# Kernel tuning notes

Measured on AMD Instinct MI355X. Metric: run time of the kernel, lower is better.

## Reference

```python
import jax, jax.numpy as jnp
import numpy as np

N_INPUT = 32
N_NEURONS = 64
N_OUTPUT = 16
BATCH = 2_000_000


def setup_inputs() -> dict:
    key = jax.random.key(0)
    k_in, k0, k1, k2 = jax.random.split(key, 4)
    inputs = jax.random.normal(k_in, (BATCH, N_INPUT), dtype=jnp.float32)
    # torch.nn.Linear(in, out, bias=False) weights have shape [out, in],
    # init U(-1/sqrt(in), 1/sqrt(in)).
    def init_w(k, fan_in, fan_out):
        b = 1.0 / np.sqrt(fan_in)
        return jax.random.uniform(k, (fan_out, fan_in), dtype=jnp.float32,
                                  minval=-b, maxval=b)
    W0 = init_w(k0, N_INPUT, N_NEURONS)     # [64, 32]
    W1 = init_w(k1, N_NEURONS, N_NEURONS)   # [64, 64]
    W2 = init_w(k2, N_NEURONS, N_OUTPUT)    # [16, 64]
    return {"inputs": inputs, "W0": W0, "W1": W1, "W2": W2}


def reference(inputs, W0, W1, W2):
    # x @ W.T for each bias-free layer, ReLU between all but the last.
    x = jax.nn.relu(jnp.einsum('bi,ni->bn', inputs, W0))
    x = jax.nn.relu(jnp.einsum('bn,mn->bm', x, W1))
    x = jnp.einsum('bm,om->bo', x, W2)
    return x
```

## Files before the change

### kernel.cpp

```cpp
#include <hip/hip_runtime.h>

typedef float f32x4 __attribute__((ext_vector_type(4)));
typedef _Float16 f16x8 __attribute__((ext_vector_type(8)));
typedef _Float16 f16x4 __attribute__((ext_vector_type(4)));
typedef int i32x4 __attribute__((ext_vector_type(4)));
typedef int i32x2 __attribute__((ext_vector_type(2)));

#define WAVES 4

__device__ __forceinline__ f32x4 mfma16(f16x8 a, f16x8 b, f32x4 c) {
    return __builtin_amdgcn_mfma_f32_16x16x32_f16(a, b, c, 0, 0, 0);
}

__device__ __forceinline__ f16x8 cvt8(f32x4 a, f32x4 b) {
    f16x8 h;
#pragma unroll
    for (int j = 0; j < 4; ++j) { h[j] = (_Float16)a[j]; h[j + 4] = (_Float16)b[j]; }
    return h;
}

__device__ __forceinline__ i32x2 relu_pk2(f32x4 a) {
    f16x4 v;
#pragma unroll
    for (int j = 0; j < 4; ++j) v[j] = (_Float16)fmaxf(a[j], 0.0f);
    return __builtin_bit_cast(i32x2, v);
}

__device__ __forceinline__ f16x8 cat(i32x2 a, i32x2 b) {
    i32x4 v; v[0] = a[0]; v[1] = a[1]; v[2] = b[0]; v[3] = b[1];
    return __builtin_bit_cast(f16x8, v);
}

__global__ __launch_bounds__(256, 4) void mlp_kernel(
    const float* __restrict__ X, const float* __restrict__ W0,
    const float* __restrict__ W1, const float* __restrict__ W2,
    float* __restrict__ Y, int ntiles)
{
    const int tid  = threadIdx.x;
    const int wid  = tid >> 6;
    const int lane = tid & 63;
    const int b16  = lane & 15;
    const int g    = lane >> 4;

    f16x8 w0[4], w1[4][2], w2[2];
#pragma unroll
    for (int t = 0; t < 4; ++t) {
        const float* p = W0 + (16 * t + b16) * 32 + 8 * g;
        w0[t] = cvt8(*(const f32x4*)p, *(const f32x4*)(p + 4));
    }
#pragma unroll
    for (int t = 0; t < 4; ++t) {
#pragma unroll
        for (int s = 0; s < 2; ++s) {
            const float* p = W1 + (16 * t + b16) * 64 + 32 * s + 4 * g;
            w1[t][s] = cvt8(*(const f32x4*)p, *(const f32x4*)(p + 16));
        }
    }
#pragma unroll
    for (int s = 0; s < 2; ++s) {
        const float* p = W2 + b16 * 64 + 32 * s + 4 * g;
        w2[s] = cvt8(*(const f32x4*)p, *(const f32x4*)(p + 16));
    }

    const int xoff = b16 * 32 + 8 * g;
    const int yoff = b16 * 16 + 4 * g;

    const int npairs = (ntiles + 1) >> 1;
    const int gwid = blockIdx.x * WAVES + wid;
    const int G    = gridDim.x * WAVES;
    if (gwid >= npairs) return;

#define LOADP(dst0, dst1, dst2, dst3, p)                                        \
    {                                                                           \
        const int pc = ((p) < npairs) ? (p) : gwid;  \
        const float* xp_ = X + (size_t)(2 * pc) * 512 + xoff;                   \
        const size_t o1_ = (2 * pc + 1 < ntiles) ? 512 : 0;                     \
        dst0 = *(const f32x4*)xp_;        dst1 = *(const f32x4*)(xp_ + 4);      \
        dst2 = *(const f32x4*)(xp_ + o1_); dst3 = *(const f32x4*)(xp_ + o1_ + 4); \
    }

#define COMPUTE_STORE(xa, p, u)                                                 \
    {                                                                           \
        i32x2 pk[4];                                                            \
        _Pragma("unroll")                                                       \
        for (int t = 0; t < 4; ++t) {                                           \
            f32x4 z = {0.f, 0.f, 0.f, 0.f};                                     \
            z = mfma16(w0[t], xa, z);                                           \
            pk[t] = relu_pk2(z);                                                \
        }                                                                       \
        f32x4 c[4];                                                             \
        _Pragma("unroll")                                                       \
        for (int t = 0; t < 4; ++t) c[t] = (f32x4){0.f, 0.f, 0.f, 0.f};         \
        const f16x8 f0 = cat(pk[0], pk[1]);                                     \
        _Pragma("unroll")                                                       \
        for (int t = 0; t < 4; ++t) c[t] = mfma16(w1[t][0], f0, c[t]);          \
        const f16x8 f1 = cat(pk[2], pk[3]);                                     \
        _Pragma("unroll")                                                       \
        for (int t = 0; t < 4; ++t) c[t] = mfma16(w1[t][1], f1, c[t]);          \
        i32x2 q[4];                                                             \
        _Pragma("unroll")                                                       \
        for (int t = 0; t < 4; ++t) q[t] = relu_pk2(c[t]);                      \
        f32x4 o = {0.f, 0.f, 0.f, 0.f};                                         \
        o = mfma16(w2[0], cat(q[0], q[1]), o);                                  \
        o = mfma16(w2[1], cat(q[2], q[3]), o);                                  \
        float* yp_ = Y + ((size_t)(2 * (p)) + (u)) * 256 + yoff;                \
        __builtin_nontemporal_store(o, (f32x4*)yp_);                            \
    }

    int p0 = gwid;
    int p1 = p0 + G;

    f32x4 a0, a1, a2, a3;
    f32x4 b0, b1, b2, b3;
    LOADP(a0, a1, a2, a3, p0)
    LOADP(b0, b1, b2, b3, p1)

    while (true) {
        {
            const f16x8 xa = cvt8(a0, a1);
            const f16x8 xb = cvt8(a2, a3);
            const int p2 = p0 + 2 * G;
            LOADP(a0, a1, a2, a3, p2)
            COMPUTE_STORE(xa, p0, 0)
            COMPUTE_STORE(xb, p0, 1)
            p0 = p2;
        }
        if (p1 >= npairs) break;

        {
            const f16x8 xa = cvt8(b0, b1);
            const f16x8 xb = cvt8(b2, b3);
            const int p3 = p1 + 2 * G;
            LOADP(b0, b1, b2, b3, p3)
            COMPUTE_STORE(xa, p1, 0)
            COMPUTE_STORE(xb, p1, 1)
            p1 = p3;
        }
        if (p0 >= npairs) break;
    }
#undef LOADP
#undef COMPUTE_STORE
}

extern "C" void kernel_launch(void* const* d_in, const int* in_sizes, int n_in,
                              void* d_out, int out_size, void* d_ws, size_t ws_size,
                              hipStream_t stream) {
    const float* X  = (const float*)d_in[0];
    const float* W0 = (const float*)d_in[1];
    const float* W1 = (const float*)d_in[2];
    const float* W2 = (const float*)d_in[3];
    float* Y = (float*)d_out;

    const int batch  = in_sizes[0] / 32;
    const int ntiles = batch / 16;
    const int npairs = (ntiles + 1) >> 1;

    int blocks = 1024;
    if (blocks * WAVES > npairs) blocks = (npairs + WAVES - 1) / WAVES;

    hipLaunchKernelGGL(mlp_kernel, dim3(blocks), dim3(256), 0, stream,
                       X, W0, W1, W2, Y, ntiles);
}
```

Baseline: 72.65 us.

## Stage W0/W1 fragments in LDS and deepen input prefetch to three pairs

Moves the fp16 W0 and W1 MFMA fragments out of registers into a shared-memory table that each wave reads per tile. The registers this frees are used to prefetch a third pair of input tiles, giving a three-stage rotation instead of two. Empty asm barriers stop the compiler from hoisting all LDS reads back into registers. The cost is extra LDS traffic and latency on every tile, in exchange for more memory loads in flight to hide HBM latency.

```diff
diff --git a/kernel.cpp b/kernel.cpp
--- a/kernel.cpp
+++ b/kernel.cpp
@@ -36,31 +36,37 @@
     const float* __restrict__ W1, const float* __restrict__ W2,
     float* __restrict__ Y, int ntiles)
 {
+    __shared__ __align__(16) _Float16 wtab[768 * 8];
+
     const int tid  = threadIdx.x;
     const int wid  = tid >> 6;
     const int lane = tid & 63;
     const int b16  = lane & 15;
     const int g    = lane >> 4;
 
-    f16x8 w0[4], w1[4][2], w2[2];
-#pragma unroll
-    for (int t = 0; t < 4; ++t) {
-        const float* p = W0 + (16 * t + b16) * 32 + 8 * g;
-        w0[t] = cvt8(*(const f32x4*)p, *(const f32x4*)(p + 4));
+    for (int e = tid; e < 768; e += 256) {
+        const int le = e & 63, b16e = le & 15, ge = le >> 4;
+        f16x8 fr;
+        if (e < 256) {
+            const int t = e >> 6;
+            const float* p = W0 + (16 * t + b16e) * 32 + 8 * ge;
+            fr = cvt8(*(const f32x4*)p, *(const f32x4*)(p + 4));
+        } else {
+            const int idx = (e - 256) >> 6, t = idx >> 1, s = idx & 1;
+            const float* p = W1 + (16 * t + b16e) * 64 + 32 * s + 4 * ge;
+            fr = cvt8(*(const f32x4*)p, *(const f32x4*)(p + 16));
+        }
+        *(f16x8*)((char*)wtab + e * 16) = fr;
     }
-#pragma unroll
-    for (int t = 0; t < 4; ++t) {
-#pragma unroll
-        for (int s = 0; s < 2; ++s) {
-            const float* p = W1 + (16 * t + b16) * 64 + 32 * s + 4 * g;
-            w1[t][s] = cvt8(*(const f32x4*)p, *(const f32x4*)(p + 16));
-        }
-    }
+
+    f16x8 w2[2];
 #pragma unroll
     for (int s = 0; s < 2; ++s) {
         const float* p = W2 + b16 * 64 + 32 * s + 4 * g;
         w2[s] = cvt8(*(const f32x4*)p, *(const f32x4*)(p + 16));
     }
+
+    __syncthreads();
 
     const int xoff = b16 * 32 + 8 * g;
     const int yoff = b16 * 16 + 4 * g;
@@ -70,76 +76,85 @@
     const int G    = gridDim.x * WAVES;
     if (gwid >= npairs) return;
 
-#define LOADP(dst0, dst1, dst2, dst3, p)                                        \
-    {                                                                           \
-        const int pc = ((p) < npairs) ? (p) : gwid;  \
-        const float* xp_ = X + (size_t)(2 * pc) * 512 + xoff;                   \
-        const size_t o1_ = (2 * pc + 1 < ntiles) ? 512 : 0;                     \
-        dst0 = *(const f32x4*)xp_;        dst1 = *(const f32x4*)(xp_ + 4);      \
-        dst2 = *(const f32x4*)(xp_ + o1_); dst3 = *(const f32x4*)(xp_ + o1_ + 4); \
+#define WFRAG(off, imm) (*(const f16x8*)((const char*)wtab + (off) + (imm)))
+
+#define LOADP(d0, d1, d2, d3, p)                                                 \
+    {                                                                            \
+        const int pc = ((p) < npairs) ? (p) : gwid;   \
+        const float* xp_ = X + (size_t)(2 * pc) * 512 + xoff;                    \
+        const size_t o1_ = (2 * pc + 1 < ntiles) ? 512 : 0;                      \
+        d0 = *(const f32x4*)xp_;          d1 = *(const f32x4*)(xp_ + 4);         \
+        d2 = *(const f32x4*)(xp_ + o1_);  d3 = *(const f32x4*)(xp_ + o1_ + 4);   \
     }
 
-#define COMPUTE_STORE(xa, p, u)                                                 \
-    {                                                                           \
-        i32x2 pk[4];                                                            \
-        _Pragma("unroll")                                                       \
-        for (int t = 0; t < 4; ++t) {                                           \
-            f32x4 z = {0.f, 0.f, 0.f, 0.f};                                     \
-            z = mfma16(w0[t], xa, z);                                           \
-            pk[t] = relu_pk2(z);                                                \
-        }                                                                       \
-        f32x4 c[4];                                                             \
-        _Pragma("unroll")                                                       \
-        for (int t = 0; t < 4; ++t) c[t] = (f32x4){0.f, 0.f, 0.f, 0.f};         \
-        const f16x8 f0 = cat(pk[0], pk[1]);                                     \
-        _Pragma("unroll")                                                       \
-        for (int t = 0; t < 4; ++t) c[t] = mfma16(w1[t][0], f0, c[t]);          \
-        const f16x8 f1 = cat(pk[2], pk[3]);                                     \
-        _Pragma("unroll")                                                       \
-        for (int t = 0; t < 4; ++t) c[t] = mfma16(w1[t][1], f1, c[t]);          \
-        i32x2 q[4];                                                             \
-        _Pragma("unroll")                                                       \
-        for (int t = 0; t < 4; ++t) q[t] = relu_pk2(c[t]);                      \
-        f32x4 o = {0.f, 0.f, 0.f, 0.f};                                         \
-        o = mfma16(w2[0], cat(q[0], q[1]), o);                                  \
-        o = mfma16(w2[1], cat(q[2], q[3]), o);                                  \
-        float* yp_ = Y + ((size_t)(2 * (p)) + (u)) * 256 + yoff;                \
-        __builtin_nontemporal_store(o, (f32x4*)yp_);                            \
+#define COMPUTE_STORE(xa, p, u)                                                  \
+    {                                                                            \
+        int o0_ = lane * 16;                                                     \
+        asm volatile("" : "+v"(o0_));                           \
+        i32x2 pk[4];                                                             \
+        _Pragma("unroll")                                                        \
+        for (int t_ = 0; t_ < 4; ++t_) {                                         \
+            f32x4 z = {0.f, 0.f, 0.f, 0.f};                                      \
+            z = mfma16(WFRAG(o0_, t_ * 1024), xa, z);                            \
+            pk[t_] = relu_pk2(z);                                                \
+        }                                                                        \
+        f32x4 c[4];                                                              \
+        _Pragma("unroll")                                                        \
+        for (int t_ = 0; t_ < 4; ++t_) c[t_] = (f32x4){0.f, 0.f, 0.f, 0.f};      \
+        int o1_ = o0_;                                                           \
+        asm volatile("" : "+v"(o1_) :: "memory");        \
+        const f16x8 f0 = cat(pk[0], pk[1]);                                      \
+        _Pragma("unroll")                                                        \
+        for (int t_ = 0; t_ < 4; ++t_)                                           \
+            c[t_] = mfma16(WFRAG(o1_, 4096 + (2 * t_) * 1024), f0, c[t_]);       \
+        int o2_ = o1_;                                                           \
+        asm volatile("" : "+v"(o2_) :: "memory");                                \
+        const f16x8 f1 = cat(pk[2], pk[3]);                                      \
+        _Pragma("unroll")                                                        \
+        for (int t_ = 0; t_ < 4; ++t_)                                           \
+            c[t_] = mfma16(WFRAG(o2_, 4096 + (2 * t_ + 1) * 1024), f1, c[t_]);   \
+        i32x2 qq[4];                                                             \
+        _Pragma("unroll")                                                        \
+        for (int t_ = 0; t_ < 4; ++t_) qq[t_] = relu_pk2(c[t_]);                 \
+        f32x4 o = {0.f, 0.f, 0.f, 0.f};                                          \
+        o = mfma16(w2[0], cat(qq[0], qq[1]), o);                                 \
+        o = mfma16(w2[1], cat(qq[2], qq[3]), o);                                 \
+        float* yp_ = Y + ((size_t)(2 * (p)) + (u)) * 256 + yoff;                 \
+        __builtin_nontemporal_store(o, (f32x4*)yp_);                             \
     }
 
-    int p0 = gwid;
-    int p1 = p0 + G;
+#define PHASE(d0, d1, d2, d3, p)                                                 \
+    {                                                                            \
+        const f16x8 xa_ = cvt8(d0, d1);                                          \
+        const f16x8 xb_ = cvt8(d2, d3);                                          \
+        const int pn_ = (p) + 3 * G;                                             \
+        LOADP(d0, d1, d2, d3, pn_)                                               \
+        COMPUTE_STORE(xa_, p, 0)                                                 \
+        COMPUTE_STORE(xb_, p, 1)                                                 \
+        p = pn_;                                                                 \
+    }
+
+    int p0 = gwid, p1 = p0 + G, p2 = p1 + G;
 
     f32x4 a0, a1, a2, a3;
     f32x4 b0, b1, b2, b3;
+    f32x4 c0, c1, c2, c3;
     LOADP(a0, a1, a2, a3, p0)
     LOADP(b0, b1, b2, b3, p1)
+    LOADP(c0, c1, c2, c3, p2)
 
     while (true) {
-        {
-            const f16x8 xa = cvt8(a0, a1);
-            const f16x8 xb = cvt8(a2, a3);
-            const int p2 = p0 + 2 * G;
-            LOADP(a0, a1, a2, a3, p2)
-            COMPUTE_STORE(xa, p0, 0)
-            COMPUTE_STORE(xb, p0, 1)
-            p0 = p2;
-        }
+        PHASE(a0, a1, a2, a3, p0)
         if (p1 >= npairs) break;
-
-        {
-            const f16x8 xa = cvt8(b0, b1);
-            const f16x8 xb = cvt8(b2, b3);
-            const int p3 = p1 + 2 * G;
-            LOADP(b0, b1, b2, b3, p3)
-            COMPUTE_STORE(xa, p1, 0)
-            COMPUTE_STORE(xb, p1, 1)
-            p1 = p3;
-        }
+        PHASE(b0, b1, b2, b3, p1)
+        if (p2 >= npairs) break;
+        PHASE(c0, c1, c2, c3, p2)
         if (p0 >= npairs) break;
     }
+#undef WFRAG
 #undef LOADP
 #undef COMPUTE_STORE
+#undef PHASE
 }
 
 extern "C" void kernel_launch(void* const* d_in, const int* in_sizes, int n_in,
```

After: 68.46 us (median of 2 runs). -5.8%, faster.
